# Performance work log

Hardware: AMD Instinct MI355X
Metric: run time of the kernel (lower is better)

The kernel has to match this reference:

```python
import jax, jax.numpy as jnp
import numpy as np

B, H, S, D = 2, 16, 2048, 128


def setup_inputs() -> dict:
    key = jax.random.key(0)
    kq, kk, kv = jax.random.split(key, 3)
    q1 = jax.random.normal(kq, (B, H, S, D), dtype=jnp.float32)
    k1 = jax.random.normal(kk, (B, H, S, D), dtype=jnp.float32)
    v1 = jax.random.normal(kv, (B, H, S, D), dtype=jnp.float32)
    scale_factor = jnp.float32(1.0 / np.sqrt(D))
    dropout_p = jnp.float32(0.5)
    return {"q1": q1, "k1": k1, "v1": v1, "scale_factor": scale_factor, "dropout_p": dropout_p}


def reference(q1, k1, v1, scale_factor, dropout_p):
    # scores: [B,H,S,S]
    qk = jnp.einsum("bhqd,bhkd->bhqk", q1, k1)
    softmax_qk = jax.nn.softmax(qk * scale_factor, axis=-1)
    # dropout (training mode, as in F.dropout default): keep w.p. 1-p, scale by 1/(1-p)
    keep = jax.random.bernoulli(jax.random.key(42), 1.0 - dropout_p, softmax_qk.shape)
    dropout_qk = jnp.where(keep, softmax_qk / (1.0 - dropout_p), 0.0)
    # output: [B,H,S,D]
    return jnp.einsum("bhqk,bhkd->bhqd", dropout_qk, v1)
```

## Files before the change

kernel.cpp:

```cpp
#include <hip/hip_runtime.h>

typedef float    f32x4  __attribute__((ext_vector_type(4)));
typedef __bf16   bf16x8 __attribute__((ext_vector_type(8)));
typedef unsigned int u32;
typedef unsigned int u32x4 __attribute__((ext_vector_type(4)));
typedef unsigned short u16;

#define S_LEN 2048
#define D_DIM 128
#define NHEAD 32
#define QBLK  128
#define KVBLK 64
#define NWAVE 8
#define WS_NEED (2u * NHEAD * S_LEN * D_DIM * 2u)

__device__ __forceinline__ u32 rotl32(u32 x, int r) {
  return __builtin_amdgcn_alignbit(x, x, 32 - r);
}

__device__ __forceinline__ u32 threefry_bits(u32 ctr) {
  const u32 ks1 = 42u;
  const u32 ks2 = 0x1BD11BF0u;
  u32 x0 = 0u;
  u32 x1 = ctr + ks1;
#define TFR(r) { x0 += x1; x1 = rotl32(x1, (r)); x1 ^= x0; }
  TFR(13) TFR(15) TFR(26) TFR(6)
  x0 += ks1; x1 += ks2 + 1u;
  TFR(17) TFR(29) TFR(16) TFR(24)
  x0 += ks2; x1 += 2u;
  TFR(13) TFR(15) TFR(26) TFR(6)
  x1 += ks1 + 3u;
  TFR(17) TFR(29) TFR(16) TFR(24)
  x0 += ks1; x1 += ks2 + 4u;
  TFR(13) TFR(15) TFR(26) TFR(6)
  x0 += ks2; x1 += 5u;
#undef TFR
  return x0 ^ x1;
}

__device__ __forceinline__ u16 f2bf(float f) {
  u32 u = __float_as_uint(f);
  return (u16)((u + 0x7fffu + ((u >> 16) & 1u)) >> 16);
}

__device__ __forceinline__ u32 cvtpk(float lo, float hi) {
  u32 r;
  asm("v_cvt_pk_bf16_f32 %0, %1, %2" : "=v"(r) : "v"(lo), "v"(hi));
  return r;
}

__device__ __forceinline__ float exp2a(float x) {
  float r;
  asm("v_exp_f32 %0, %1" : "=v"(r) : "v"(x));
  return r;
}

__device__ __forceinline__ void gl_lds16(const void* g, void* l) {
  __builtin_amdgcn_global_load_lds(
      (const __attribute__((address_space(1))) void*)g,
      (__attribute__((address_space(3))) void*)l, 16, 0, 0);
}

__device__ __forceinline__ u32 swzv(int d) { return (u32)((d & 7) ^ ((d >> 2) & 7)); }

__global__ void __launch_bounds__(256) prepack(
    const float* __restrict__ Kp, const float* __restrict__ Vp,
    u16* __restrict__ kimg, u16* __restrict__ vimg)
{
  __shared__ u16 vt[KVBLK * D_DIM];
  const int blk = blockIdx.x;
  const int h = blk >> 5, tk = blk & 31;
  const float* Kh = Kp + ((size_t)h * S_LEN + (size_t)tk * KVBLK) * D_DIM;
  const float* Vh = Vp + ((size_t)h * S_LEN + (size_t)tk * KVBLK) * D_DIM;
  u16* kd = kimg + (size_t)blk * (KVBLK * D_DIM);
  u16* vd = vimg + (size_t)blk * (KVBLK * D_DIM);
  const int t = threadIdx.x;

#pragma unroll
  for (int it = 0; it < 4; ++it) {
    u32 p = (u32)(it * 256 + t) * 16;
    u32 krow = p >> 8;
    u32 cb = (p & 255) ^ ((krow & 7) << 4);
    const float* src = Kh + krow * D_DIM + (cb >> 1);
    f32x4 a = *(const f32x4*)(src);
    f32x4 b = *(const f32x4*)(src + 4);
    u32x4 o;
    o.x = cvtpk(a[0], a[1]); o.y = cvtpk(a[2], a[3]);
    o.z = cvtpk(b[0], b[1]); o.w = cvtpk(b[2], b[3]);
    *(u32x4*)((char*)kd + p) = o;
  }
#pragma unroll
  for (int it = 0; it < 8; ++it) {
    int g = it * 256 + t;
    int kv = g >> 5, d4 = g & 31;
    f32x4 x = *(const f32x4*)(Vh + (size_t)kv * D_DIM + d4 * 4);
    u32* dst = (u32*)(vt + kv * D_DIM + d4 * 4);
    dst[0] = cvtpk(x[0], x[1]);
    dst[1] = cvtpk(x[2], x[3]);
  }
  __syncthreads();
#pragma unroll
  for (int it = 0; it < 4; ++it) {
    u32 p = (u32)(it * 256 + t) * 16;
    u32 vdr = p >> 7;
    u32 cb = (p & 127) ^ (swzv((int)vdr) << 4);
    u32 kv0 = cb >> 1;
    u16 e[8];
#pragma unroll
    for (int i = 0; i < 8; ++i) e[i] = vt[(kv0 + i) * D_DIM + vdr];
    u32x4 o;
    o.x = (u32)e[0] | ((u32)e[1] << 16);
    o.y = (u32)e[2] | ((u32)e[3] << 16);
    o.z = (u32)e[4] | ((u32)e[5] << 16);
    o.w = (u32)e[6] | ((u32)e[7] << 16);
    *(u32x4*)((char*)vd + p) = o;
  }
}

__global__ void __launch_bounds__(512, 4) attn_fwd(
    const float* __restrict__ Qp, const u16* __restrict__ kimg,
    const u16* __restrict__ vimg, const float* __restrict__ scp,
    const float* __restrict__ dpp, float* __restrict__ Op)
{
  __shared__ alignas(16) u16 kbuf[KVBLK * D_DIM];
  __shared__ alignas(16) u16 vbuf[D_DIM * KVBLK];
  __shared__ alignas(16) u16 pbuf[NWAVE][16 * KVBLK];

  const int n    = blockIdx.x;
  const int head = ((n & 7) << 2) | ((n >> 3) & 3);
  const int qblk = n >> 5;
  const int t  = threadIdx.x;
  const int w  = t >> 6;
  const int l  = t & 63;
  const int lg = l >> 4;
  const int lc = l & 15;

  const float scale  = scp[0];
  const float keep_p = 1.0f - dpp[0];
  const float qmul   = scale * 1.44269504088896340736f;

  u32 ithr;
  {
    float T = keep_p * 8388608.0f;
    u32 Ti = (u32)T;
    u32 thr9 = ((float)Ti == T) ? Ti : (Ti + 1u);
    ithr = (thr9 >= (1u << 23)) ? 0xFFFFFFFFu : (thr9 << 9);
  }

  const float* __restrict__ Qh = Qp + (size_t)head * (S_LEN * D_DIM);
  float*       __restrict__ Oh = Op + (size_t)head * (S_LEN * D_DIM);
  const u16* __restrict__ kim = kimg + (size_t)head * 32 * (KVBLK * D_DIM);
  const u16* __restrict__ vim = vimg + (size_t)head * 32 * (KVBLK * D_DIM);

  bf16x8 qf[4];
  {
    const int qrow = qblk * QBLK + w * 16 + lc;
    const float* qsrc = Qh + (size_t)qrow * D_DIM + lg * 8;
#pragma unroll
    for (int kc = 0; kc < 4; ++kc) {
      f32x4 a = *(const f32x4*)(qsrc + kc * 32);
      f32x4 b = *(const f32x4*)(qsrc + kc * 32 + 4);
      union { u32 w4[4]; bf16x8 v; } uu;
      uu.w4[0] = cvtpk(a[0] * qmul, a[1] * qmul);
      uu.w4[1] = cvtpk(a[2] * qmul, a[3] * qmul);
      uu.w4[2] = cvtpk(b[0] * qmul, b[1] * qmul);
      uu.w4[3] = cvtpk(b[2] * qmul, b[3] * qmul);
      qf[kc] = uu.v;
    }
  }

  f32x4 acc[8];
#pragma unroll
  for (int dt = 0; dt < 8; ++dt) acc[dt] = f32x4{0.f, 0.f, 0.f, 0.f};
  float lrun[4] = { 0.f, 0.f, 0.f, 0.f };

  u16* pb = &pbuf[w][0];
  const u32 qrow_c0 = (u32)(qblk * QBLK + w * 16 + lg * 4);
  const u32 ibase0  = ((u32)head * S_LEN + qrow_c0) * S_LEN;

  for (int tkv = 0; tkv < S_LEN / KVBLK; ++tkv) {
    {
      const u16* kt_ = kim + (size_t)tkv * (KVBLK * D_DIM);
      const u16* vt_ = vim + (size_t)tkv * (KVBLK * D_DIM);
#pragma unroll
      for (int it = 0; it < 2; ++it) {
        int ck = it * 8 + w;
        gl_lds16((const char*)kt_ + ck * 1024 + l * 16, (char*)kbuf + ck * 1024);
        gl_lds16((const char*)vt_ + ck * 1024 + l * 16, (char*)vbuf + ck * 1024);
      }
    }
    __syncthreads();

    f32x4 sa[4];
#pragma unroll
    for (int ct = 0; ct < 4; ++ct) sa[ct] = f32x4{0.f, 0.f, 0.f, 0.f};
#pragma unroll
    for (int kc = 0; kc < 4; ++kc) {
#pragma unroll
      for (int ct = 0; ct < 4; ++ct) {
        int krow = ct * 16 + lc;
        u32 koff = ((u32)(krow * 256 + (lg * 8 + kc * 32) * 2)) ^ ((u32)(krow & 7) << 4);
        bf16x8 kf = *(const bf16x8*)((char*)kbuf + koff);
        sa[ct] = __builtin_amdgcn_mfma_f32_16x16x32_bf16(qf[kc], kf, sa[ct], 0, 0, 0);
      }
    }

#pragma unroll
    for (int j = 0; j < 4; ++j) {
      u32 ib = ibase0 + (u32)j * S_LEN + (u32)(tkv * KVBLK) + (u32)lc;
      float p0 = exp2a(sa[0][j]);
      float p1 = exp2a(sa[1][j]);
      float p2 = exp2a(sa[2][j]);
      float p3 = exp2a(sa[3][j]);
      lrun[j] += (p0 + p1) + (p2 + p3);
      u32 b0 = threefry_bits(ib);
      u32 b1 = threefry_bits(ib + 16u);
      u32 b2 = threefry_bits(ib + 32u);
      u32 b3 = threefry_bits(ib + 48u);
      float m0 = (b0 < ithr) ? p0 : 0.0f;
      float m1 = (b1 < ithr) ? p1 : 0.0f;
      float m2 = (b2 < ithr) ? p2 : 0.0f;
      float m3 = (b3 < ithr) ? p3 : 0.0f;
      u32 pk01 = cvtpk(m0, m1);
      u32 pk23 = cvtpk(m2, m3);
      int prow = lg * 4 + j;
      u32 rb = (u32)(prow * 128 + lc * 2);
      u32 sw = (u32)(prow & 7) << 4;
      *(u16*)((char*)pb + ((rb      ) ^ sw)) = (u16)pk01;
      *(u16*)((char*)pb + ((rb +  32) ^ sw)) = (u16)(pk01 >> 16);
      *(u16*)((char*)pb + ((rb +  64) ^ sw)) = (u16)pk23;
      *(u16*)((char*)pb + ((rb +  96) ^ sw)) = (u16)(pk23 >> 16);
    }

#pragma unroll
    for (int kc2 = 0; kc2 < 2; ++kc2) {
      u32 poff = ((u32)(lc * 128 + (lg * 8 + kc2 * 32) * 2)) ^ ((u32)(lc & 7) << 4);
      bf16x8 pa = *(const bf16x8*)((char*)pb + poff);
#pragma unroll
      for (int dt = 0; dt < 8; ++dt) {
        int vd = dt * 16 + lc;
        u32 voff = ((u32)(vd * 128 + (lg * 8 + kc2 * 32) * 2)) ^ (swzv(vd) << 4);
        bf16x8 vb = *(const bf16x8*)((char*)vbuf + voff);
        acc[dt] = __builtin_amdgcn_mfma_f32_16x16x32_bf16(pa, vb, acc[dt], 0, 0, 0);
      }
    }
    __syncthreads();
  }

#pragma unroll
  for (int j = 0; j < 4; ++j) {
    float ls = lrun[j];
    ls += __shfl_xor(ls, 1, 64);
    ls += __shfl_xor(ls, 2, 64);
    ls += __shfl_xor(ls, 4, 64);
    ls += __shfl_xor(ls, 8, 64);
    float sc = (1.0f / keep_p) / ls;
    u32 qg = qrow_c0 + (u32)j;
#pragma unroll
    for (int dt = 0; dt < 8; ++dt) {
      Oh[(size_t)qg * D_DIM + dt * 16 + lc] = acc[dt][j] * sc;
    }
  }
}

__global__ void __launch_bounds__(256) attn_fwd_fb(
    const float* __restrict__ Qp, const float* __restrict__ Kp,
    const float* __restrict__ Vp, const float* __restrict__ scp,
    const float* __restrict__ dpp, float* __restrict__ Op)
{
  __shared__ alignas(16) u16 kbuf[KVBLK * D_DIM];
  __shared__ alignas(16) u16 vbuf[D_DIM * KVBLK];
  __shared__ alignas(16) u16 pbuf[4][16 * KVBLK];

  const int n    = blockIdx.y * gridDim.x + blockIdx.x;
  const int head = ((n & 7) << 2) | ((n >> 3) & 3);
  const int qblk = n >> 5;
  const int t  = threadIdx.x;
  const int w  = t >> 6;
  const int l  = t & 63;
  const int lg = l >> 4;
  const int lc = l & 15;

  const float scale  = scp[0];
  const float keep_p = 1.0f - dpp[0];
  const float qmul   = scale * 1.44269504088896340736f;
  u32 ithr;
  {
    float T = keep_p * 8388608.0f;
    u32 Ti = (u32)T;
    u32 thr9 = ((float)Ti == T) ? Ti : (Ti + 1u);
    ithr = (thr9 >= (1u << 23)) ? 0xFFFFFFFFu : (thr9 << 9);
  }

  const float* __restrict__ Qh = Qp + (size_t)head * (S_LEN * D_DIM);
  const float* __restrict__ Kh = Kp + (size_t)head * (S_LEN * D_DIM);
  const float* __restrict__ Vh = Vp + (size_t)head * (S_LEN * D_DIM);
  float*       __restrict__ Oh = Op + (size_t)head * (S_LEN * D_DIM);

  bf16x8 qf[4];
  {
    const int qrow = qblk * 64 + w * 16 + lc;
    const float* qsrc = Qh + (size_t)qrow * D_DIM + lg * 8;
#pragma unroll
    for (int kc = 0; kc < 4; ++kc) {
      f32x4 a = *(const f32x4*)(qsrc + kc * 32);
      f32x4 b = *(const f32x4*)(qsrc + kc * 32 + 4);
      union { u16 h[8]; bf16x8 v; } uu;
#pragma unroll
      for (int i = 0; i < 4; ++i) {
        uu.h[i]     = f2bf(a[i] * qmul);
        uu.h[4 + i] = f2bf(b[i] * qmul);
      }
      qf[kc] = uu.v;
    }
  }

  f32x4 acc[8];
#pragma unroll
  for (int dt = 0; dt < 8; ++dt) acc[dt] = f32x4{0.f, 0.f, 0.f, 0.f};
  float lrun[4] = { 0.f, 0.f, 0.f, 0.f };

  u16* pb = &pbuf[w][0];
  const u32 qrow_c0 = (u32)(qblk * 64 + w * 16 + lg * 4);
  const u32 ibase0  = ((u32)head * S_LEN + qrow_c0) * S_LEN;

  for (int tkv = 0; tkv < S_LEN / KVBLK; ++tkv) {
#pragma unroll
    for (int r = 0; r < 8; ++r) {
      int g = r * 256 + t;
      int kv = g >> 5, d4 = g & 31;
      f32x4 x = *(const f32x4*)(Kh + (size_t)(tkv * KVBLK + kv) * D_DIM + d4 * 4);
      u32 w0 = (u32)f2bf(x[0]) | ((u32)f2bf(x[1]) << 16);
      u32 w1 = (u32)f2bf(x[2]) | ((u32)f2bf(x[3]) << 16);
      u32 off = ((u32)(kv * 256 + d4 * 8)) ^ ((u32)(kv & 7) << 4);
      u32* dst = (u32*)((char*)kbuf + off);
      dst[0] = w0; dst[1] = w1;
    }
#pragma unroll
    for (int r = 0; r < 8; ++r) {
      int rowloc = w * 16 + (r & 1) * 8 + (l >> 3);
      int d4     = (r >> 1) * 8 + (l & 7);
      f32x4 x = *(const f32x4*)(Vh + (size_t)(tkv * KVBLK + rowloc) * D_DIM + d4 * 4);
      u16 mb0 = f2bf(x[0]), mb1 = f2bf(x[1]), mb2 = f2bf(x[2]), mb3 = f2bf(x[3]);
      u16 pb0 = (u16)__shfl_xor((int)mb0, 8, 64);
      u16 pb1 = (u16)__shfl_xor((int)mb1, 8, 64);
      u16 pb2 = (u16)__shfl_xor((int)mb2, 8, 64);
      u16 pb3 = (u16)__shfl_xor((int)mb3, 8, 64);
      bool ev = ((l >> 3) & 1) == 0;
      int kvp = rowloc & ~1;
      u32 wA = ev ? ((u32)mb0 | ((u32)pb0 << 16)) : ((u32)pb2 | ((u32)mb2 << 16));
      u32 wB = ev ? ((u32)mb1 | ((u32)pb1 << 16)) : ((u32)pb3 | ((u32)mb3 << 16));
      int dA = d4 * 4 + (ev ? 0 : 2);
      u32 offA = ((u32)(dA * 128 + kvp * 2)) ^ (swzv(dA) << 4);
      u32 offB = ((u32)((dA + 1) * 128 + kvp * 2)) ^ (swzv(dA + 1) << 4);
      *(u32*)((char*)vbuf + offA) = wA;
      *(u32*)((char*)vbuf + offB) = wB;
    }
    __syncthreads();

    f32x4 sa[4];
#pragma unroll
    for (int ct = 0; ct < 4; ++ct) sa[ct] = f32x4{0.f, 0.f, 0.f, 0.f};
#pragma unroll
    for (int kc = 0; kc < 4; ++kc) {
#pragma unroll
      for (int ct = 0; ct < 4; ++ct) {
        int krow = ct * 16 + lc;
        u32 koff = ((u32)(krow * 256 + (lg * 8 + kc * 32) * 2)) ^ ((u32)(krow & 7) << 4);
        bf16x8 kf = *(const bf16x8*)((char*)kbuf + koff);
        sa[ct] = __builtin_amdgcn_mfma_f32_16x16x32_bf16(qf[kc], kf, sa[ct], 0, 0, 0);
      }
    }

#pragma unroll
    for (int j = 0; j < 4; ++j) {
      u32 ib = ibase0 + (u32)j * S_LEN + (u32)(tkv * KVBLK) + (u32)lc;
      float p0 = exp2a(sa[0][j]);
      float p1 = exp2a(sa[1][j]);
      float p2 = exp2a(sa[2][j]);
      float p3 = exp2a(sa[3][j]);
      lrun[j] += (p0 + p1) + (p2 + p3);
      u32 b0 = threefry_bits(ib);
      u32 b1 = threefry_bits(ib + 16u);
      u32 b2 = threefry_bits(ib + 32u);
      u32 b3 = threefry_bits(ib + 48u);
      float m0 = (b0 < ithr) ? p0 : 0.0f;
      float m1 = (b1 < ithr) ? p1 : 0.0f;
      float m2 = (b2 < ithr) ? p2 : 0.0f;
      float m3 = (b3 < ithr) ? p3 : 0.0f;
      u32 pk01 = cvtpk(m0, m1);
      u32 pk23 = cvtpk(m2, m3);
      int prow = lg * 4 + j;
      u32 rb = (u32)(prow * 128 + lc * 2);
      u32 sw = (u32)(prow & 7) << 4;
      *(u16*)((char*)pb + ((rb      ) ^ sw)) = (u16)pk01;
      *(u16*)((char*)pb + ((rb +  32) ^ sw)) = (u16)(pk01 >> 16);
      *(u16*)((char*)pb + ((rb +  64) ^ sw)) = (u16)pk23;
      *(u16*)((char*)pb + ((rb +  96) ^ sw)) = (u16)(pk23 >> 16);
    }

#pragma unroll
    for (int kc2 = 0; kc2 < 2; ++kc2) {
      u32 poff = ((u32)(lc * 128 + (lg * 8 + kc2 * 32) * 2)) ^ ((u32)(lc & 7) << 4);
      bf16x8 pa = *(const bf16x8*)((char*)pb + poff);
#pragma unroll
      for (int dt = 0; dt < 8; ++dt) {
        int vd = dt * 16 + lc;
        u32 voff = ((u32)(vd * 128 + (lg * 8 + kc2 * 32) * 2)) ^ (swzv(vd) << 4);
        bf16x8 vb = *(const bf16x8*)((char*)vbuf + voff);
        acc[dt] = __builtin_amdgcn_mfma_f32_16x16x32_bf16(pa, vb, acc[dt], 0, 0, 0);
      }
    }
    __syncthreads();
  }

#pragma unroll
  for (int j = 0; j < 4; ++j) {
    float ls = lrun[j];
    ls += __shfl_xor(ls, 1, 64);
    ls += __shfl_xor(ls, 2, 64);
    ls += __shfl_xor(ls, 4, 64);
    ls += __shfl_xor(ls, 8, 64);
    float sc = (1.0f / keep_p) / ls;
    u32 qg = qrow_c0 + (u32)j;
#pragma unroll
    for (int dt = 0; dt < 8; ++dt) {
      Oh[(size_t)qg * D_DIM + dt * 16 + lc] = acc[dt][j] * sc;
    }
  }
}

extern "C" void kernel_launch(void* const* d_in, const int* in_sizes, int n_in,
                              void* d_out, int out_size, void* d_ws, size_t ws_size,
                              hipStream_t stream) {
  const float* q  = (const float*)d_in[0];
  const float* k  = (const float*)d_in[1];
  const float* v  = (const float*)d_in[2];
  const float* sc = (const float*)d_in[3];
  const float* dp = (const float*)d_in[4];
  float* out = (float*)d_out;
  if (ws_size >= (size_t)WS_NEED) {
    u16* kimg = (u16*)d_ws;
    u16* vimg = kimg + (size_t)NHEAD * S_LEN * D_DIM;
    hipLaunchKernelGGL(prepack, dim3(NHEAD * (S_LEN / KVBLK)), dim3(256), 0, stream, k, v, kimg, vimg);
    hipLaunchKernelGGL(attn_fwd, dim3(NHEAD * (S_LEN / QBLK)), dim3(512), 0, stream,
                       q, kimg, vimg, sc, dp, out);
  } else {
    hipLaunchKernelGGL(attn_fwd_fb, dim3(S_LEN / 64, NHEAD), dim3(256), 0, stream, q, k, v, sc, dp, out);
  }
}
```

Measured before the change: 323.5 us.

## Stage two KV tiles per barrier pair and raise wave priority around MFMA

The main attention kernel now stages two K/V tiles into separate LDS buffers before one barrier, then computes both tiles, halving the number of __syncthreads per KV sweep. It also wraps the MFMA sections in s_setprio and adds a scheduling barrier and compiler memory fences around the P-tile LDS writes and reads. Doubling K/V LDS use may reduce occupancy below the four blocks per CU requested by launch bounds. Loads are still not overlapped with compute, since both stages complete before either compute begins.

After: 384.6 us. 18.9% more time.

```diff
diff --git a/kernel.cpp b/kernel.cpp
--- a/kernel.cpp
+++ b/kernel.cpp
@@ -13,6 +13,8 @@
 #define KVBLK 64
 #define NWAVE 8
 #define WS_NEED (2u * NHEAD * S_LEN * D_DIM * 2u)
+
+#define MEMFENCE() asm volatile("" ::: "memory")
 
 __device__ __forceinline__ u32 rotl32(u32 x, int r) {
   return __builtin_amdgcn_alignbit(x, x, 32 - r);
@@ -122,8 +124,8 @@
     const u16* __restrict__ vimg, const float* __restrict__ scp,
     const float* __restrict__ dpp, float* __restrict__ Op)
 {
-  __shared__ alignas(16) u16 kbuf[KVBLK * D_DIM];
-  __shared__ alignas(16) u16 vbuf[D_DIM * KVBLK];
+  __shared__ alignas(16) u16 kbuf[2][KVBLK * D_DIM];
+  __shared__ alignas(16) u16 vbuf[2][D_DIM * KVBLK];
   __shared__ alignas(16) u16 pbuf[NWAVE][16 * KVBLK];
 
   const int n    = blockIdx.x;
@@ -178,16 +180,199 @@
   const u32 qrow_c0 = (u32)(qblk * QBLK + w * 16 + lg * 4);
   const u32 ibase0  = ((u32)head * S_LEN + qrow_c0) * S_LEN;
 
+#define STAGE_TILE(BUF, TKV)                                                      \
+  {                                                                               \
+    const u16* kt_ = kim + (size_t)(TKV) * (KVBLK * D_DIM);                       \
+    const u16* vt_ = vim + (size_t)(TKV) * (KVBLK * D_DIM);                       \
+    _Pragma("unroll")                                                             \
+    for (int it = 0; it < 2; ++it) {                                              \
+      int ck = it * 8 + w;                                                        \
+      gl_lds16((const char*)kt_ + ck * 1024 + l * 16, (char*)kbuf[BUF] + ck * 1024); \
+      gl_lds16((const char*)vt_ + ck * 1024 + l * 16, (char*)vbuf[BUF] + ck * 1024); \
+    }                                                                             \
+  }
+
+#define COMPUTE_TILE(BUF, TKV)                                                    \
+  {                                                                               \
+    f32x4 sa[4];                                                                  \
+    _Pragma("unroll")                                                             \
+    for (int ct = 0; ct < 4; ++ct) sa[ct] = f32x4{0.f, 0.f, 0.f, 0.f};            \
+    __builtin_amdgcn_s_setprio(1);                                                \
+    _Pragma("unroll")                                                             \
+    for (int kc = 0; kc < 4; ++kc) {                                              \
+      _Pragma("unroll")                                                           \
+      for (int ct = 0; ct < 4; ++ct) {                                            \
+        int krow = ct * 16 + lc;                                                  \
+        u32 koff = ((u32)(krow * 256 + (lg * 8 + kc * 32) * 2)) ^ ((u32)(krow & 7) << 4); \
+        bf16x8 kf = *(const bf16x8*)((char*)kbuf[BUF] + koff);                    \
+        sa[ct] = __builtin_amdgcn_mfma_f32_16x16x32_bf16(qf[kc], kf, sa[ct], 0, 0, 0); \
+      }                                                                           \
+    }                                                                             \
+    __builtin_amdgcn_s_setprio(0);                                                \
+    _Pragma("unroll")                                                             \
+    for (int j = 0; j < 4; ++j) {                                                 \
+      u32 ib = ibase0 + (u32)j * S_LEN + (u32)((TKV) * KVBLK) + (u32)lc;          \
+      float p0 = exp2a(sa[0][j]);                                                 \
+      float p1 = exp2a(sa[1][j]);                                                 \
+      float p2 = exp2a(sa[2][j]);                                                 \
+      float p3 = exp2a(sa[3][j]);                                                 \
+      lrun[j] += (p0 + p1) + (p2 + p3);                                           \
+      u32 b0 = threefry_bits(ib);                                                 \
+      u32 b1 = threefry_bits(ib + 16u);                                           \
+      u32 b2 = threefry_bits(ib + 32u);                                           \
+      u32 b3 = threefry_bits(ib + 48u);                                           \
+      float m0 = (b0 < ithr) ? p0 : 0.0f;                                         \
+      float m1 = (b1 < ithr) ? p1 : 0.0f;                                         \
+      float m2 = (b2 < ithr) ? p2 : 0.0f;                                         \
+      float m3 = (b3 < ithr) ? p3 : 0.0f;                                         \
+      u32 pk01 = cvtpk(m0, m1);                                                   \
+      u32 pk23 = cvtpk(m2, m3);                                                   \
+      int prow = lg * 4 + j;                                                      \
+      u32 rb = (u32)(prow * 128 + lc * 2);                                        \
+      u32 sw = (u32)(prow & 7) << 4;                                              \
+      *(u16*)((char*)pb + ((rb      ) ^ sw)) = (u16)pk01;                         \
+      *(u16*)((char*)pb + ((rb +  32) ^ sw)) = (u16)(pk01 >> 16);                 \
+      *(u16*)((char*)pb + ((rb +  64) ^ sw)) = (u16)pk23;                         \
+      *(u16*)((char*)pb + ((rb +  96) ^ sw)) = (u16)(pk23 >> 16);                 \
+    }                                                                             \
+    MEMFENCE();                                                                   \
+    __builtin_amdgcn_sched_barrier(0);                                            \
+    __builtin_amdgcn_s_setprio(1);                                                \
+    _Pragma("unroll")                                                             \
+    for (int kc2 = 0; kc2 < 2; ++kc2) {                                           \
+      u32 poff = ((u32)(lc * 128 + (lg * 8 + kc2 * 32) * 2)) ^ ((u32)(lc & 7) << 4); \
+      bf16x8 pa = *(const bf16x8*)((char*)pb + poff);                             \
+      _Pragma("unroll")                                                           \
+      for (int dt = 0; dt < 8; ++dt) {                                            \
+        int vd = dt * 16 + lc;                                                    \
+        u32 voff = ((u32)(vd * 128 + (lg * 8 + kc2 * 32) * 2)) ^ (swzv(vd) << 4); \
+        bf16x8 vb = *(const bf16x8*)((char*)vbuf[BUF] + voff);                    \
+        acc[dt] = __builtin_amdgcn_mfma_f32_16x16x32_bf16(pa, vb, acc[dt], 0, 0, 0); \
+      }                                                                           \
+    }                                                                             \
+    __builtin_amdgcn_s_setprio(0);                                                \
+    MEMFENCE();                                                                   \
+  }
+
+  for (int tkv = 0; tkv < S_LEN / KVBLK; tkv += 2) {
+    STAGE_TILE(0, tkv)
+    STAGE_TILE(1, tkv + 1)
+    __syncthreads();
+    COMPUTE_TILE(0, tkv)
+    COMPUTE_TILE(1, tkv + 1)
+    __syncthreads();
+  }
+#undef STAGE_TILE
+#undef COMPUTE_TILE
+
+#pragma unroll
+  for (int j = 0; j < 4; ++j) {
+    float ls = lrun[j];
+    ls += __shfl_xor(ls, 1, 64);
+    ls += __shfl_xor(ls, 2, 64);
+    ls += __shfl_xor(ls, 4, 64);
+    ls += __shfl_xor(ls, 8, 64);
+    float sc = (1.0f / keep_p) / ls;
+    u32 qg = qrow_c0 + (u32)j;
+#pragma unroll
+    for (int dt = 0; dt < 8; ++dt) {
+      Oh[(size_t)qg * D_DIM + dt * 16 + lc] = acc[dt][j] * sc;
+    }
+  }
+}
+
+__global__ void __launch_bounds__(256) attn_fwd_fb(
+    const float* __restrict__ Qp, const float* __restrict__ Kp,
+    const float* __restrict__ Vp, const float* __restrict__ scp,
+    const float* __restrict__ dpp, float* __restrict__ Op)
+{
+  __shared__ alignas(16) u16 kbuf[KVBLK * D_DIM];
+  __shared__ alignas(16) u16 vbuf[D_DIM * KVBLK];
+  __shared__ alignas(16) u16 pbuf[4][16 * KVBLK];
+
+  const int n    = blockIdx.y * gridDim.x + blockIdx.x;
+  const int head = ((n & 7) << 2) | ((n >> 3) & 3);
+  const int qblk = n >> 5;
+  const int t  = threadIdx.x;
+  const int w  = t >> 6;
+  const int l  = t & 63;
+  const int lg = l >> 4;
+  const int lc = l & 15;
+
+  const float scale  = scp[0];
+  const float keep_p = 1.0f - dpp[0];
+  const float qmul   = scale * 1.44269504088896340736f;
+  u32 ithr;
+  {
+    float T = keep_p * 8388608.0f;
+    u32 Ti = (u32)T;
+    u32 thr9 = ((float)Ti == T) ? Ti : (Ti + 1u);
+    ithr = (thr9 >= (1u << 23)) ? 0xFFFFFFFFu : (thr9 << 9);
+  }
+
+  const float* __restrict__ Qh = Qp + (size_t)head * (S_LEN * D_DIM);
+  const float* __restrict__ Kh = Kp + (size_t)head * (S_LEN * D_DIM);
+  const float* __restrict__ Vh = Vp + (size_t)head * (S_LEN * D_DIM);
+  float*       __restrict__ Oh = Op + (size_t)head * (S_LEN * D_DIM);
+
+  bf16x8 qf[4];
+  {
+    const int qrow = qblk * 64 + w * 16 + lc;
+    const float* qsrc = Qh + (size_t)qrow * D_DIM + lg * 8;
+#pragma unroll
+    for (int kc = 0; kc < 4; ++kc) {
+      f32x4 a = *(const f32x4*)(qsrc + kc * 32);
+      f32x4 b = *(const f32x4*)(qsrc + kc * 32 + 4);
+      union { u16 h[8]; bf16x8 v; } uu;
+#pragma unroll
+      for (int i = 0; i < 4; ++i) {
+        uu.h[i]     = f2bf(a[i] * qmul);
+        uu.h[4 + i] = f2bf(b[i] * qmul);
+      }
+      qf[kc] = uu.v;
+    }
+  }
+
+  f32x4 acc[8];
+#pragma unroll
+  for (int dt = 0; dt < 8; ++dt) acc[dt] = f32x4{0.f, 0.f, 0.f, 0.f};
+  float lrun[4] = { 0.f, 0.f, 0.f, 0.f };
+
+  u16* pb = &pbuf[w][0];
+  const u32 qrow_c0 = (u32)(qblk * 64 + w * 16 + lg * 4);
+  const u32 ibase0  = ((u32)head * S_LEN + qrow_c0) * S_LEN;
+
   for (int tkv = 0; tkv < S_LEN / KVBLK; ++tkv) {
-    {
-      const u16* kt_ = kim + (size_t)tkv * (KVBLK * D_DIM);
-      const u16* vt_ = vim + (size_t)tkv * (KVBLK * D_DIM);
-#pragma unroll
-      for (int it = 0; it < 2; ++it) {
-        int ck = it * 8 + w;
-        gl_lds16((const char*)kt_ + ck * 1024 + l * 16, (char*)kbuf + ck * 1024);
-        gl_lds16((const char*)vt_ + ck * 1024 + l * 16, (char*)vbuf + ck * 1024);
-      }
+#pragma unroll
+    for (int r = 0; r < 8; ++r) {
+      int g = r * 256 + t;
+      int kv = g >> 5, d4 = g & 31;
+      f32x4 x = *(const f32x4*)(Kh + (size_t)(tkv * KVBLK + kv) * D_DIM + d4 * 4);
+      u32 w0 = (u32)f2bf(x[0]) | ((u32)f2bf(x[1]) << 16);
+      u32 w1 = (u32)f2bf(x[2]) | ((u32)f2bf(x[3]) << 16);
+      u32 off = ((u32)(kv * 256 + d4 * 8)) ^ ((u32)(kv & 7) << 4);
+      u32* dst = (u32*)((char*)kbuf + off);
+      dst[0] = w0; dst[1] = w1;
+    }
+#pragma unroll
+    for (int r = 0; r < 8; ++r) {
+      int rowloc = w * 16 + (r & 1) * 8 + (l >> 3);
+      int d4     = (r >> 1) * 8 + (l & 7);
+      f32x4 x = *(const f32x4*)(Vh + (size_t)(tkv * KVBLK + rowloc) * D_DIM + d4 * 4);
+      u16 mb0 = f2bf(x[0]), mb1 = f2bf(x[1]), mb2 = f2bf(x[2]), mb3 = f2bf(x[3]);
+      u16 pb0 = (u16)__shfl_xor((int)mb0, 8, 64);
+      u16 pb1 = (u16)__shfl_xor((int)mb1, 8, 64);
+      u16 pb2 = (u16)__shfl_xor((int)mb2, 8, 64);
+      u16 pb3 = (u16)__shfl_xor((int)mb3, 8, 64);
+      bool ev = ((l >> 3) & 1) == 0;
+      int kvp = rowloc & ~1;
+      u32 wA = ev ? ((u32)mb0 | ((u32)pb0 << 16)) : ((u32)pb2 | ((u32)mb2 << 16));
+      u32 wB = ev ? ((u32)mb1 | ((u32)pb1 << 16)) : ((u32)pb3 | ((u32)mb3 << 16));
+      int dA = d4 * 4 + (ev ? 0 : 2);
+      u32 offA = ((u32)(dA * 128 + kvp * 2)) ^ (swzv(dA) << 4);
+      u32 offB = ((u32)((dA + 1) * 128 + kvp * 2)) ^ (swzv(dA + 1) << 4);
+      *(u32*)((char*)vbuf + offA) = wA;
+      *(u32*)((char*)vbuf + offB) = wB;
     }
     __syncthreads();
 
@@ -231,6 +416,7 @@
       *(u16*)((char*)pb + ((rb +  64) ^ sw)) = (u16)pk23;
       *(u16*)((char*)pb + ((rb +  96) ^ sw)) = (u16)(pk23 >> 16);
     }
+    asm volatile("" ::: "memory");
 
 #pragma unroll
     for (int kc2 = 0; kc2 < 2; ++kc2) {
@@ -244,173 +430,7 @@
         acc[dt] = __builtin_amdgcn_mfma_f32_16x16x32_bf16(pa, vb, acc[dt], 0, 0, 0);
       }
     }
-    __syncthreads();
-  }
-
-#pragma unroll
-  for (int j = 0; j < 4; ++j) {
-    float ls = lrun[j];
-    ls += __shfl_xor(ls, 1, 64);
-    ls += __shfl_xor(ls, 2, 64);
-    ls += __shfl_xor(ls, 4, 64);
-    ls += __shfl_xor(ls, 8, 64);
-    float sc = (1.0f / keep_p) / ls;
-    u32 qg = qrow_c0 + (u32)j;
-#pragma unroll
-    for (int dt = 0; dt < 8; ++dt) {
-      Oh[(size_t)qg * D_DIM + dt * 16 + lc] = acc[dt][j] * sc;
-    }
-  }
-}
-
-__global__ void __launch_bounds__(256) attn_fwd_fb(
-    const float* __restrict__ Qp, const float* __restrict__ Kp,
-    const float* __restrict__ Vp, const float* __restrict__ scp,
-    const float* __restrict__ dpp, float* __restrict__ Op)
-{
-  __shared__ alignas(16) u16 kbuf[KVBLK * D_DIM];
-  __shared__ alignas(16) u16 vbuf[D_DIM * KVBLK];
-  __shared__ alignas(16) u16 pbuf[4][16 * KVBLK];
-
-  const int n    = blockIdx.y * gridDim.x + blockIdx.x;
-  const int head = ((n & 7) << 2) | ((n >> 3) & 3);
-  const int qblk = n >> 5;
-  const int t  = threadIdx.x;
-  const int w  = t >> 6;
-  const int l  = t & 63;
-  const int lg = l >> 4;
-  const int lc = l & 15;
-
-  const float scale  = scp[0];
-  const float keep_p = 1.0f - dpp[0];
-  const float qmul   = scale * 1.44269504088896340736f;
-  u32 ithr;
-  {
-    float T = keep_p * 8388608.0f;
-    u32 Ti = (u32)T;
-    u32 thr9 = ((float)Ti == T) ? Ti : (Ti + 1u);
-    ithr = (thr9 >= (1u << 23)) ? 0xFFFFFFFFu : (thr9 << 9);
-  }
-
-  const float* __restrict__ Qh = Qp + (size_t)head * (S_LEN * D_DIM);
-  const float* __restrict__ Kh = Kp + (size_t)head * (S_LEN * D_DIM);
-  const float* __restrict__ Vh = Vp + (size_t)head * (S_LEN * D_DIM);
-  float*       __restrict__ Oh = Op + (size_t)head * (S_LEN * D_DIM);
-
-  bf16x8 qf[4];
-  {
-    const int qrow = qblk * 64 + w * 16 + lc;
-    const float* qsrc = Qh + (size_t)qrow * D_DIM + lg * 8;
-#pragma unroll
-    for (int kc = 0; kc < 4; ++kc) {
-      f32x4 a = *(const f32x4*)(qsrc + kc * 32);
-      f32x4 b = *(const f32x4*)(qsrc + kc * 32 + 4);
-      union { u16 h[8]; bf16x8 v; } uu;
-#pragma unroll
-      for (int i = 0; i < 4; ++i) {
-        uu.h[i]     = f2bf(a[i] * qmul);
-        uu.h[4 + i] = f2bf(b[i] * qmul);
-      }
-      qf[kc] = uu.v;
-    }
-  }
-
-  f32x4 acc[8];
-#pragma unroll
-  for (int dt = 0; dt < 8; ++dt) acc[dt] = f32x4{0.f, 0.f, 0.f, 0.f};
-  float lrun[4] = { 0.f, 0.f, 0.f, 0.f };
-
-  u16* pb = &pbuf[w][0];
-  const u32 qrow_c0 = (u32)(qblk * 64 + w * 16 + lg * 4);
-  const u32 ibase0  = ((u32)head * S_LEN + qrow_c0) * S_LEN;
-
-  for (int tkv = 0; tkv < S_LEN / KVBLK; ++tkv) {
-#pragma unroll
-    for (int r = 0; r < 8; ++r) {
-      int g = r * 256 + t;
-      int kv = g >> 5, d4 = g & 31;
-      f32x4 x = *(const f32x4*)(Kh + (size_t)(tkv * KVBLK + kv) * D_DIM + d4 * 4);
-      u32 w0 = (u32)f2bf(x[0]) | ((u32)f2bf(x[1]) << 16);
-      u32 w1 = (u32)f2bf(x[2]) | ((u32)f2bf(x[3]) << 16);
-      u32 off = ((u32)(kv * 256 + d4 * 8)) ^ ((u32)(kv & 7) << 4);
-      u32* dst = (u32*)((char*)kbuf + off);
-      dst[0] = w0; dst[1] = w1;
-    }
-#pragma unroll
-    for (int r = 0; r < 8; ++r) {
-      int rowloc = w * 16 + (r & 1) * 8 + (l >> 3);
-      int d4     = (r >> 1) * 8 + (l & 7);
-      f32x4 x = *(const f32x4*)(Vh + (size_t)(tkv * KVBLK + rowloc) * D_DIM + d4 * 4);
-      u16 mb0 = f2bf(x[0]), mb1 = f2bf(x[1]), mb2 = f2bf(x[2]), mb3 = f2bf(x[3]);
-      u16 pb0 = (u16)__shfl_xor((int)mb0, 8, 64);
-      u16 pb1 = (u16)__shfl_xor((int)mb1, 8, 64);
-      u16 pb2 = (u16)__shfl_xor((int)mb2, 8, 64);
-      u16 pb3 = (u16)__shfl_xor((int)mb3, 8, 64);
-      bool ev = ((l >> 3) & 1) == 0;
-      int kvp = rowloc & ~1;
-      u32 wA = ev ? ((u32)mb0 | ((u32)pb0 << 16)) : ((u32)pb2 | ((u32)mb2 << 16));
-      u32 wB = ev ? ((u32)mb1 | ((u32)pb1 << 16)) : ((u32)pb3 | ((u32)mb3 << 16));
-      int dA = d4 * 4 + (ev ? 0 : 2);
-      u32 offA = ((u32)(dA * 128 + kvp * 2)) ^ (swzv(dA) << 4);
-      u32 offB = ((u32)((dA + 1) * 128 + kvp * 2)) ^ (swzv(dA + 1) << 4);
-      *(u32*)((char*)vbuf + offA) = wA;
-      *(u32*)((char*)vbuf + offB) = wB;
-    }
-    __syncthreads();
-
-    f32x4 sa[4];
-#pragma unroll
-    for (int ct = 0; ct < 4; ++ct) sa[ct] = f32x4{0.f, 0.f, 0.f, 0.f};
-#pragma unroll
-    for (int kc = 0; kc < 4; ++kc) {
-#pragma unroll
-      for (int ct = 0; ct < 4; ++ct) {
-        int krow = ct * 16 + lc;
-        u32 koff = ((u32)(krow * 256 + (lg * 8 + kc * 32) * 2)) ^ ((u32)(krow & 7) << 4);
-        bf16x8 kf = *(const bf16x8*)((char*)kbuf + koff);
-        sa[ct] = __builtin_amdgcn_mfma_f32_16x16x32_bf16(qf[kc], kf, sa[ct], 0, 0, 0);
-      }
-    }
-
-#pragma unroll
-    for (int j = 0; j < 4; ++j) {
-      u32 ib = ibase0 + (u32)j * S_LEN + (u32)(tkv * KVBLK) + (u32)lc;
-      float p0 = exp2a(sa[0][j]);
-      float p1 = exp2a(sa[1][j]);
-      float p2 = exp2a(sa[2][j]);
-      float p3 = exp2a(sa[3][j]);
-      lrun[j] += (p0 + p1) + (p2 + p3);
-      u32 b0 = threefry_bits(ib);
-      u32 b1 = threefry_bits(ib + 16u);
-      u32 b2 = threefry_bits(ib + 32u);
-      u32 b3 = threefry_bits(ib + 48u);
-      float m0 = (b0 < ithr) ? p0 : 0.0f;
-      float m1 = (b1 < ithr) ? p1 : 0.0f;
-      float m2 = (b2 < ithr) ? p2 : 0.0f;
-      float m3 = (b3 < ithr) ? p3 : 0.0f;
-      u32 pk01 = cvtpk(m0, m1);
-      u32 pk23 = cvtpk(m2, m3);
-      int prow = lg * 4 + j;
-      u32 rb = (u32)(prow * 128 + lc * 2);
-      u32 sw = (u32)(prow & 7) << 4;
-      *(u16*)((char*)pb + ((rb      ) ^ sw)) = (u16)pk01;
-      *(u16*)((char*)pb + ((rb +  32) ^ sw)) = (u16)(pk01 >> 16);
-      *(u16*)((char*)pb + ((rb +  64) ^ sw)) = (u16)pk23;
-      *(u16*)((char*)pb + ((rb +  96) ^ sw)) = (u16)(pk23 >> 16);
-    }
-
-#pragma unroll
-    for (int kc2 = 0; kc2 < 2; ++kc2) {
-      u32 poff = ((u32)(lc * 128 + (lg * 8 + kc2 * 32) * 2)) ^ ((u32)(lc & 7) << 4);
-      bf16x8 pa = *(const bf16x8*)((char*)pb + poff);
-#pragma unroll
-      for (int dt = 0; dt < 8; ++dt) {
-        int vd = dt * 16 + lc;
-        u32 voff = ((u32)(vd * 128 + (lg * 8 + kc2 * 32) * 2)) ^ (swzv(vd) << 4);
-        bf16x8 vb = *(const bf16x8*)((char*)vbuf + voff);
-        acc[dt] = __builtin_amdgcn_mfma_f32_16x16x32_bf16(pa, vb, acc[dt], 0, 0, 0);
-      }
-    }
+    asm volatile("" ::: "memory");
     __syncthreads();
   }
 
```
